# Kernel tuning notes

Measured on AMD Instinct MI355X. Metric: run time of the kernel, lower is better.

The kernel has to match this reference:

```python
import jax, jax.numpy as jnp
import numpy as np

N = 100000
E = 1600000
G = 256
D_IN = 128
NEURON = 64
ATT_F = 8
K = 3
ALPHA = 0.1


def setup_inputs() -> dict:
    key = jax.random.key(0)
    ks = jax.random.split(key, 12)
    x = jax.random.normal(ks[0], (N, D_IN), dtype=jnp.float32)
    closeness_feature = jax.random.normal(ks[1], (N, ATT_F), dtype=jnp.float32)
    edge_index = jax.random.randint(ks[2], (2, E), 0, N, dtype=jnp.int32)
    batch = jnp.sort(jax.random.randint(ks[3], (N,), 0, G, dtype=jnp.int32))
    s = 0.05
    return {
        "x": x,
        "closeness_feature": closeness_feature,
        "edge_index": edge_index,
        "batch": batch,
        "num_graphs": G,
        "nn1_w": jax.random.normal(ks[4], (D_IN, NEURON), dtype=jnp.float32) * s,
        "nn1_b": jnp.zeros((NEURON,), dtype=jnp.float32),
        "close_w": jax.random.normal(ks[5], (ATT_F, 1), dtype=jnp.float32) * s,
        "close_b": jnp.zeros((1,), dtype=jnp.float32),
        "att1_w": jax.random.normal(ks[6], (NEURON, 16), dtype=jnp.float32) * s,
        "att1_b": jnp.zeros((16,), dtype=jnp.float32),
        "att2_w": jax.random.normal(ks[7], (16, 1), dtype=jnp.float32) * s,
        "att2_b": jnp.zeros((1,), dtype=jnp.float32),
    }


def _appnp(x, edge_index, n):
    # gcn_norm with self-loops: A_hat = D^{-1/2}(A+I)D^{-1/2}
    loop = jnp.arange(n, dtype=edge_index.dtype)
    src = jnp.concatenate([edge_index[0], loop])
    dst = jnp.concatenate([edge_index[1], loop])
    deg = jax.ops.segment_sum(jnp.ones_like(dst, dtype=x.dtype), dst, num_segments=n)
    dinv = jax.lax.rsqrt(deg)  # deg >= 1 due to self loops
    norm = (dinv[src] * dinv[dst])[:, None]  # [E+N, 1]
    h = x
    for _ in range(K):
        agg = jax.ops.segment_sum(norm * h[src], dst, num_segments=n)
        h = (1.0 - ALPHA) * agg + ALPHA * x
    return h


def reference(x, closeness_feature, edge_index, batch, num_graphs,
              nn1_w, nn1_b, close_w, close_b, att1_w, att1_b, att2_w, att2_b):
    n = x.shape[0]
    h = _appnp(x, edge_index, n)                      # [N, D_IN]
    h = jax.nn.relu(h @ nn1_w + nn1_b)                # [N, 64]

    # per-graph softmax over closeness scores (segment softmax)
    logits = (closeness_feature @ close_w + close_b)[:, 0]          # [N]
    m = jax.ops.segment_max(logits, batch, num_segments=num_graphs)  # [G]
    w = jnp.exp(logits - m[batch])
    z = jax.ops.segment_sum(w, batch, num_segments=num_graphs)       # [G]
    p = w / z[batch]                                                 # softmax per graph

    cnt = jax.ops.segment_sum(jnp.ones((n,), dtype=h.dtype), batch,
                              num_segments=num_graphs)               # nodes per graph
    p = p * cnt[batch]                                               # scaled by curr_size

    # self_max: per-graph max over weighted node features
    pooled = jax.ops.segment_max(p[:, None] * h, batch, num_segments=num_graphs)  # [G, 64]

    a = jax.nn.relu(pooled @ att1_w + att1_b)         # [G, 16]
    return a @ att2_w + att2_b                        # [G, 1]
```

## Files before the change

### kernel.cpp

```cpp
#include <hip/hip_runtime.h>
#include <cstdint>
#include <cstddef>


#define DIN 128
#define NEU 64
#define BK2 512
#define BKSHIFT2 9
#define BKCAP 16384
#define ESCAP 12288
#define MAXNB 256

typedef __attribute__((ext_vector_type(8))) short short8v;
typedef __attribute__((ext_vector_type(4))) float f32x4;

__device__ inline float bf2f(unsigned short h) {
    return __uint_as_float(((unsigned)h) << 16);
}
__device__ inline unsigned short f2bf(float f) {
    unsigned u = __float_as_uint(f);
    unsigned r = u + 0x7FFFu + ((u >> 16) & 1u);
    return (unsigned short)(r >> 16);
}


__global__ __launch_bounds__(256) void binA_kernel(
        const int* __restrict__ src, const int* __restrict__ dst,
        int* __restrict__ bcur, int* __restrict__ pk, int E, int NB) {
    __shared__ int hist[MAXNB];
    __shared__ int cur[MAXNB];
    int nchunk = gridDim.x;
    int chunk = (E + nchunk - 1) / nchunk;
    int lo = blockIdx.x * chunk;
    int hi = min(E, lo + chunk);
    int t = threadIdx.x;
    for (int b = t; b < NB; b += 256) hist[b] = 0;
    __syncthreads();
    for (int i = lo + t; i < hi; i += 256)
        atomicAdd(&hist[dst[i] >> BKSHIFT2], 1);
    __syncthreads();
    for (int b = t; b < NB; b += 256)
        cur[b] = atomicAdd(&bcur[b], hist[b]);
    __syncthreads();
    for (int i = lo + t; i < hi; i += 256) {
        int d = dst[i];
        int b = d >> BKSHIFT2;
        int pos = atomicAdd(&cur[b], 1);
        pk[(size_t)b * BKCAP + pos] = (src[i] << BKSHIFT2) | (d & (BK2 - 1));
    }
}


__global__ void bscan_kernel(const int* __restrict__ bcur, int* __restrict__ bbase, int NB) {
    __shared__ int sh[256];
    int t = threadIdx.x;
    sh[t] = (t < NB) ? bcur[t] : 0;
    __syncthreads();
    for (int d = 1; d < 256; d <<= 1) {
        int v = (t >= d) ? sh[t - d] : 0;
        __syncthreads();
        sh[t] += v;
        __syncthreads();
    }
    if (t < NB) bbase[t + 1] = sh[t];
    if (t == 0) bbase[0] = 0;
}


__global__ __launch_bounds__(256) void binB_kernel(
        const int* __restrict__ bcur, const int* __restrict__ bbase,
        const int* __restrict__ pk, int* __restrict__ es,
        int* __restrict__ rowptr, float* __restrict__ dinv, int N, int NB) {
    __shared__ int cur[BK2];
    __shared__ int sh[256];
    __shared__ int esl[ESCAP];
    int b = blockIdx.x;
    int t = threadIdx.x;
    int node0 = b << BKSHIFT2;
    int count = bcur[b];
    int base = bbase[b];
    const int* pb = pk + (size_t)b * BKCAP;

    for (int v = t; v < BK2; v += 256) cur[v] = 0;
    __syncthreads();
    for (int i = t; i < count; i += 256)
        atomicAdd(&cur[pb[i] & (BK2 - 1)], 1);
    __syncthreads();
    int c0 = cur[2 * t], c1 = cur[2 * t + 1];
    int s = c0 + c1;
    sh[t] = s;
    __syncthreads();
    for (int d = 1; d < 256; d <<= 1) {
        int v = (t >= d) ? sh[t - d] : 0;
        __syncthreads();
        sh[t] += v;
        __syncthreads();
    }
    int excl = sh[t] - s;
    int n0 = node0 + 2 * t;
    if (n0 < N) {
        rowptr[n0 + 1] = base + excl + c0;
        dinv[n0] = rsqrtf((float)c0 + 1.0f);
    }
    if (n0 + 1 < N) {
        rowptr[n0 + 2] = base + excl + c0 + c1;
        dinv[n0 + 1] = rsqrtf((float)c1 + 1.0f);
    }
    if (b == 0 && t == 0) rowptr[0] = 0;
    __syncthreads();
    cur[2 * t] = excl;
    cur[2 * t + 1] = excl + c0;
    __syncthreads();
    for (int i = t; i < count; i += 256) {
        int v = pb[i];
        int pos = atomicAdd(&cur[v & (BK2 - 1)], 1);
        if (pos < ESCAP) esl[pos] = v >> BKSHIFT2;
    }
    __syncthreads();
    for (int i = t; i < count; i += 256) es[base + i] = esl[i];
}


__global__ __launch_bounds__(256) void fc1_kernel(
        const float* __restrict__ x, const float* __restrict__ W,
        const float* __restrict__ dinv, ushort* __restrict__ yb,
        ushort* __restrict__ g0, ushort* __restrict__ g1,
        ushort* __restrict__ g2, int N) {
    int tid = threadIdx.x;
    if (blockIdx.x == 0 && tid < 48) {
        int buf = tid >> 4, e = tid & 15;
        ushort* gp = (buf == 0) ? g0 : (buf == 1) ? g1 : g2;
        ((ushort4*)(gp + (size_t)N * NEU))[e] = make_ushort4(0, 0, 0, 0);
    }
    __shared__ ushort sW[DIN * NEU];
    for (int k = tid; k < DIN * NEU / 2; k += 256) {
        float2 v = ((const float2*)W)[k];
        ushort2 o;
        o.x = f2bf(v.x);
        o.y = f2bf(v.y);
        ((ushort2*)sW)[k] = o;
    }
    __syncthreads();
    int lane = tid & 63;
    int wv = tid >> 6;
    int l15 = lane & 15;
    int lg = lane >> 4;
    short8v bfrag[4][4];
#pragma unroll
    for (int kt = 0; kt < 4; kt++)
#pragma unroll
        for (int ct = 0; ct < 4; ct++) {
            short8v f;
#pragma unroll
            for (int e = 0; e < 8; e++)
                f[e] = (short)sW[(kt * 32 + lg * 8 + e) * NEU + ct * 16 + l15];
            bfrag[kt][ct] = f;
        }
    long long row0 = (long long)blockIdx.x * 64 + wv * 16;
    if (row0 >= N) return;
    bool rowok = (row0 + l15) < N;
    const float* xr = x + (size_t)(row0 + l15) * DIN;
    f32x4 acc[4];
#pragma unroll
    for (int ct = 0; ct < 4; ct++) acc[ct] = (f32x4){0.f, 0.f, 0.f, 0.f};
#pragma unroll
    for (int kt = 0; kt < 4; kt++) {
        short8v af = (short8v){0, 0, 0, 0, 0, 0, 0, 0};
        if (rowok) {
            float4 v0 = *((const float4*)(xr + kt * 32 + lg * 8));
            float4 v1 = *((const float4*)(xr + kt * 32 + lg * 8 + 4));
            af[0] = (short)f2bf(v0.x); af[1] = (short)f2bf(v0.y);
            af[2] = (short)f2bf(v0.z); af[3] = (short)f2bf(v0.w);
            af[4] = (short)f2bf(v1.x); af[5] = (short)f2bf(v1.y);
            af[6] = (short)f2bf(v1.z); af[7] = (short)f2bf(v1.w);
        }
#pragma unroll
        for (int ct = 0; ct < 4; ct++)
            acc[ct] = __builtin_amdgcn_mfma_f32_16x16x32_bf16(af, bfrag[kt][ct], acc[ct], 0, 0, 0);
    }
#pragma unroll
    for (int r = 0; r < 4; r++) {
        long long rr = row0 + lg * 4 + r;
        if (rr < N) {
            float dv = dinv[rr];
#pragma unroll
            for (int ct = 0; ct < 4; ct++) {
                float v = acc[ct][r];
                yb[(size_t)rr * NEU + ct * 16 + l15] = f2bf(v);
                g0[(size_t)rr * NEU + ct * 16 + l15] = f2bf(dv * v);
            }
        }
    }
}


template <int MODE>
__global__ __launch_bounds__(256) void pull_kernel(
        const int* __restrict__ rowptr, const int* __restrict__ es,
        const float* __restrict__ dinv, const ushort* __restrict__ gin,
        const ushort* __restrict__ yb, const float* __restrict__ b1,
        ushort* __restrict__ gout, float* __restrict__ h2out, int N) {
    int wid = threadIdx.x >> 6;
    int lane = threadIdx.x & 63;
    int quarter = lane >> 4;
    int l16 = lane & 15;
    int node = blockIdx.x * 4 + wid;
    if (node >= N) return;
    int beg = rowptr[node], end = rowptr[node + 1];
    float dd = dinv[node];
    const ushort4* gin4 = (const ushort4*)gin;
    float4 a0 = make_float4(0.f, 0.f, 0.f, 0.f);
    float4 a1 = make_float4(0.f, 0.f, 0.f, 0.f);
    int deg = end - beg;
    for (int base = 0; base < deg; base += 64) {
        int myi = base + lane;
        int msrc = (myi < deg) ? es[beg + myi] : N;
        int cnt = min(64, deg - base);
        int quads = (cnt + 3) >> 2;
        int j = 0;
        for (; j + 1 < quads; j += 2) {
            int s0 = __shfl(msrc, 4 * j + quarter);
            int s1 = __shfl(msrc, 4 * j + 4 + quarter);
            ushort4 w0 = gin4[(uint)(s0 << 4) + l16];
            ushort4 w1 = gin4[(uint)(s1 << 4) + l16];
            a0.x += bf2f(w0.x); a0.y += bf2f(w0.y); a0.z += bf2f(w0.z); a0.w += bf2f(w0.w);
            a1.x += bf2f(w1.x); a1.y += bf2f(w1.y); a1.z += bf2f(w1.z); a1.w += bf2f(w1.w);
        }
        if (j < quads) {
            int s0 = __shfl(msrc, 4 * j + quarter);
            ushort4 w0 = gin4[(uint)(s0 << 4) + l16];
            a0.x += bf2f(w0.x); a0.y += bf2f(w0.y); a0.z += bf2f(w0.z); a0.w += bf2f(w0.w);
        }
    }
    float4 acc;
    acc.x = a0.x + a1.x;
    acc.y = a0.y + a1.y;
    acc.z = a0.z + a1.z;
    acc.w = a0.w + a1.w;
    acc.x += __shfl_xor(acc.x, 16);
    acc.y += __shfl_xor(acc.y, 16);
    acc.z += __shfl_xor(acc.z, 16);
    acc.w += __shfl_xor(acc.w, 16);
    acc.x += __shfl_xor(acc.x, 32);
    acc.y += __shfl_xor(acc.y, 32);
    acc.z += __shfl_xor(acc.z, 32);
    acc.w += __shfl_xor(acc.w, 32);
    if (quarter == 0) {
        ushort4 gv = *((const ushort4*)(gin + (size_t)node * NEU) + l16);
        ushort4 yv = *((const ushort4*)(yb + (size_t)node * NEU) + l16);
        float c9 = 0.9f * dd;
        float hx = c9 * (acc.x + bf2f(gv.x)) + 0.1f * bf2f(yv.x);
        float hy = c9 * (acc.y + bf2f(gv.y)) + 0.1f * bf2f(yv.y);
        float hz = c9 * (acc.z + bf2f(gv.z)) + 0.1f * bf2f(yv.z);
        float hw = c9 * (acc.w + bf2f(gv.w)) + 0.1f * bf2f(yv.w);
        if (MODE == 1) {
            float4 bb = *((const float4*)b1 + l16);
            float4 o;
            o.x = fmaxf(hx + bb.x, 0.f);
            o.y = fmaxf(hy + bb.y, 0.f);
            o.z = fmaxf(hz + bb.z, 0.f);
            o.w = fmaxf(hw + bb.w, 0.f);
            *((float4*)(h2out + (size_t)node * NEU) + l16) = o;
        } else {
            ushort4 o;
            o.x = f2bf(dd * hx); o.y = f2bf(dd * hy);
            o.z = f2bf(dd * hz); o.w = f2bf(dd * hw);
            *((ushort4*)(gout + (size_t)node * NEU) + l16) = o;
        }
    }
}


__global__ __launch_bounds__(256) void head_kernel(
        const int* __restrict__ batch, const float* __restrict__ cf,
        const float* __restrict__ cw, const float* __restrict__ cb,
        const float* __restrict__ h2, const float* __restrict__ aw1,
        const float* __restrict__ ab1, const float* __restrict__ aw2,
        const float* __restrict__ ab2, float* __restrict__ out, int N) {
    int g = blockIdx.x;
    int tid = threadIdx.x;
    __shared__ int sbound[2];
    __shared__ float redm[256];
    __shared__ float redz[256];
    __shared__ float pooled[64];
    __shared__ float sa[16];
    if (tid < 2) {
        int target = g + tid;
        int lo = 0, hi = N;
        while (lo < hi) {
            int mid = (lo + hi) >> 1;
            if (batch[mid] < target) lo = mid + 1; else hi = mid;
        }
        sbound[tid] = lo;
    }
    __syncthreads();
    int s0 = sbound[0], e0 = sbound[1];
    float w0 = cw[0], w1 = cw[1], w2 = cw[2], w3 = cw[3];
    float w4 = cw[4], w5 = cw[5], w6 = cw[6], w7 = cw[7];
    float cb0 = cb[0];
    float m = -INFINITY, z = 0.f;
    for (int i = s0 + tid; i < e0; i += 256) {
        const float4* c = (const float4*)(cf + (size_t)i * 8);
        float4 A = c[0], B = c[1];
        float l = A.x * w0 + A.y * w1 + A.z * w2 + A.w * w3
                + B.x * w4 + B.y * w5 + B.z * w6 + B.w * w7 + cb0;
        float mn = fmaxf(m, l);
        z = z * __expf(m - mn) + __expf(l - mn);
        m = mn;
    }
    redm[tid] = m; redz[tid] = z;
    __syncthreads();
    for (int w = 128; w > 0; w >>= 1) {
        if (tid < w) {
            float ma = redm[tid], mb = redm[tid + w];
            float za = redz[tid], zb = redz[tid + w];
            float mn = fmaxf(ma, mb);
            redz[tid] = (mn == -INFINITY) ? 0.f
                       : za * __expf(ma - mn) + zb * __expf(mb - mn);
            redm[tid] = mn;
        }
        __syncthreads();
    }
    float M = redm[0];
    float scale = (float)(e0 - s0) / redz[0];
    __syncthreads();
    int j = tid & 63, r = tid >> 6;
    float mx = -INFINITY;
    for (int i = s0 + r; i < e0; i += 4) {
        const float4* c = (const float4*)(cf + (size_t)i * 8);
        float4 A = c[0], B = c[1];
        float l = A.x * w0 + A.y * w1 + A.z * w2 + A.w * w3
                + B.x * w4 + B.y * w5 + B.z * w6 + B.w * w7 + cb0;
        float p = __expf(l - M) * scale;
        mx = fmaxf(mx, p * h2[(size_t)i * NEU + j]);
    }
    redm[tid] = mx;
    __syncthreads();
    if (r == 0)
        pooled[j] = fmaxf(fmaxf(redm[j], redm[64 + j]),
                          fmaxf(redm[128 + j], redm[192 + j]));
    __syncthreads();
    if (tid < 16) {
        float acc = ab1[tid];
#pragma unroll
        for (int k = 0; k < 64; k++) acc = fmaf(pooled[k], aw1[k * 16 + tid], acc);
        sa[tid] = fmaxf(acc, 0.f);
    }
    __syncthreads();
    if (tid == 0) {
        float o = ab2[0];
#pragma unroll
        for (int k = 0; k < 16; k++) o = fmaf(sa[k], aw2[k], o);
        out[g] = o;
    }
}


extern "C" void kernel_launch(void* const* d_in, const int* in_sizes, int n_in,
                              void* d_out, int out_size, void* d_ws, size_t ws_size,
                              hipStream_t stream) {
    const float* x       = (const float*)d_in[0];
    const float* cf      = (const float*)d_in[1];
    const int*   ei      = (const int*)d_in[2];
    const int*   batch   = (const int*)d_in[3];
    const float* nn1_w   = (const float*)d_in[5];
    const float* nn1_b   = (const float*)d_in[6];
    const float* close_w = (const float*)d_in[7];
    const float* close_b = (const float*)d_in[8];
    const float* att1_w  = (const float*)d_in[9];
    const float* att1_b  = (const float*)d_in[10];
    const float* att2_w  = (const float*)d_in[11];
    const float* att2_b  = (const float*)d_in[12];
    float* out = (float*)d_out;

    int N = in_sizes[0] / DIN;
    int E = in_sizes[2] / 2;
    int G = out_size;

    const int* src = ei;
    const int* dst = ei + E;

    char* w = (char*)d_ws;
    size_t off = 0;
    auto alloc = [&](size_t bytes) -> void* {
        void* ptr = w + off;
        off += (bytes + 511) & ~(size_t)511;
        return ptr;
    };
    int NB = (N + BK2 - 1) >> BKSHIFT2;

    ushort* yb     = (ushort*)alloc((size_t)N * NEU * 2);
    ushort* g0     = (ushort*)alloc(((size_t)N + 1) * NEU * 2);
    ushort* g1     = (ushort*)alloc(((size_t)N + 1) * NEU * 2);
    ushort* g2     = (ushort*)alloc(((size_t)N + 1) * NEU * 2);
    float* h2      = (float*)alloc((size_t)N * NEU * 4);
    float* dinv    = (float*)alloc((size_t)N * 4);
    int*   rowptr  = (int*)alloc(((size_t)N + 1) * 4);
    int*   es      = (int*)alloc((size_t)E * 4);
    int*   bcur    = (int*)alloc((size_t)NB * 4);
    int*   bbase   = (int*)alloc(((size_t)NB + 1) * 4);
    int*   pk      = (int*)alloc((size_t)NB * BKCAP * 4);
    (void)ws_size; (void)n_in;

    hipMemsetAsync(bcur, 0, (size_t)NB * 4, stream);

    binA_kernel<<<256, 256, 0, stream>>>(src, dst, bcur, pk, E, NB);
    bscan_kernel<<<1, 256, 0, stream>>>(bcur, bbase, NB);
    binB_kernel<<<NB, 256, 0, stream>>>(bcur, bbase, pk, es, rowptr, dinv, N, NB);

    fc1_kernel<<<(N + 63) / 64, 256, 0, stream>>>(x, nn1_w, dinv, yb, g0, g1, g2, N);

    pull_kernel<0><<<(N + 3) / 4, 256, 0, stream>>>(rowptr, es, dinv, g0, yb, nn1_b, g1, nullptr, N);
    pull_kernel<0><<<(N + 3) / 4, 256, 0, stream>>>(rowptr, es, dinv, g1, yb, nn1_b, g2, nullptr, N);
    pull_kernel<1><<<(N + 3) / 4, 256, 0, stream>>>(rowptr, es, dinv, g2, yb, nn1_b, nullptr, h2, N);

    head_kernel<<<G, 256, 0, stream>>>(batch, cf, close_w, close_b, h2,
                                       att1_w, att1_b, att2_w, att2_b, out, N);
}
```

Baseline: 242.7 us.

## Stage binned edges in LDS, fold bucket scan into binB, unroll pull by four

binA now computes a local prefix over its bucket histogram and stages packed edges in shared memory sorted by bucket. It then writes them to global memory in bucket-contiguous runs, aiming for more coalesced scattered writes. The separate bscan kernel is removed and every binB block recomputes the prefix over bucket counts itself, which saves one launch at the cost of redundant scans. The pull kernel's gather loop is unrolled to four independent loads and accumulators for more memory-level parallelism. The risk is that ASTAGE=6400 must cover the per-block chunk (E/256=6250), and the extra shared memory may reduce occupancy.

```diff
diff --git a/kernel.cpp b/kernel.cpp
--- a/kernel.cpp
+++ b/kernel.cpp
@@ -10,6 +10,7 @@
 #define BKCAP 16384
 #define ESCAP 12288
 #define MAXNB 256
+#define ASTAGE 6400
 
 typedef __attribute__((ext_vector_type(8))) short short8v;
 typedef __attribute__((ext_vector_type(4))) float f32x4;
@@ -28,7 +29,12 @@
         const int* __restrict__ src, const int* __restrict__ dst,
         int* __restrict__ bcur, int* __restrict__ pk, int E, int NB) {
     __shared__ int hist[MAXNB];
-    __shared__ int cur[MAXNB];
+    __shared__ int lstart[MAXNB];
+    __shared__ int lcur[MAXNB];
+    __shared__ int resv[MAXNB];
+    __shared__ int sh[256];
+    __shared__ int stage[ASTAGE];
+    __shared__ int gidx[ASTAGE];
     int nchunk = gridDim.x;
     int chunk = (E + nchunk - 1) / nchunk;
     int lo = blockIdx.x * chunk;
@@ -39,61 +45,75 @@
     for (int i = lo + t; i < hi; i += 256)
         atomicAdd(&hist[dst[i] >> BKSHIFT2], 1);
     __syncthreads();
-    for (int b = t; b < NB; b += 256)
-        cur[b] = atomicAdd(&bcur[b], hist[b]);
+    int c = (t < NB) ? hist[t] : 0;
+    sh[t] = c;
+    __syncthreads();
+    for (int d = 1; d < 256; d <<= 1) {
+        int u = (t >= d) ? sh[t - d] : 0;
+        __syncthreads();
+        sh[t] += u;
+        __syncthreads();
+    }
+    if (t < NB) {
+        int excl = sh[t] - c;
+        lstart[t] = excl;
+        lcur[t] = excl;
+        resv[t] = atomicAdd(&bcur[t], c);
+    }
     __syncthreads();
     for (int i = lo + t; i < hi; i += 256) {
-        int d = dst[i];
-        int b = d >> BKSHIFT2;
-        int pos = atomicAdd(&cur[b], 1);
-        pk[(size_t)b * BKCAP + pos] = (src[i] << BKSHIFT2) | (d & (BK2 - 1));
-    }
-}
-
-
-__global__ void bscan_kernel(const int* __restrict__ bcur, int* __restrict__ bbase, int NB) {
-    __shared__ int sh[256];
-    int t = threadIdx.x;
-    sh[t] = (t < NB) ? bcur[t] : 0;
-    __syncthreads();
-    for (int d = 1; d < 256; d <<= 1) {
-        int v = (t >= d) ? sh[t - d] : 0;
-        __syncthreads();
-        sh[t] += v;
-        __syncthreads();
-    }
-    if (t < NB) bbase[t + 1] = sh[t];
-    if (t == 0) bbase[0] = 0;
+        int d = dst[i], b = d >> BKSHIFT2;
+        int p = atomicAdd(&lcur[b], 1);
+        stage[p] = (src[i] << BKSHIFT2) | (d & (BK2 - 1));
+        gidx[p] = resv[b] + (p - lstart[b]) + b * BKCAP;
+    }
+    __syncthreads();
+    int total = hi - lo;
+    for (int q = t; q < total; q += 256)
+        pk[gidx[q]] = stage[q];
 }
 
 
 __global__ __launch_bounds__(256) void binB_kernel(
-        const int* __restrict__ bcur, const int* __restrict__ bbase,
-        const int* __restrict__ pk, int* __restrict__ es,
-        int* __restrict__ rowptr, float* __restrict__ dinv, int N, int NB) {
+        const int* __restrict__ bcur, const int* __restrict__ pk,
+        int* __restrict__ es, int* __restrict__ rowptr,
+        float* __restrict__ dinv, int N, int NB) {
     __shared__ int cur[BK2];
     __shared__ int sh[256];
     __shared__ int esl[ESCAP];
+    __shared__ int sbase[2];
     int b = blockIdx.x;
     int t = threadIdx.x;
     int node0 = b << BKSHIFT2;
-    int count = bcur[b];
-    int base = bbase[b];
+    int v = (t < NB) ? bcur[t] : 0;
+    sh[t] = v;
+    __syncthreads();
+    for (int d = 1; d < 256; d <<= 1) {
+        int u = (t >= d) ? sh[t - d] : 0;
+        __syncthreads();
+        sh[t] += u;
+        __syncthreads();
+    }
+    if (t == b) { sbase[0] = sh[t] - v; sbase[1] = v; }
+    __syncthreads();
+    int base = sbase[0];
+    int count = sbase[1];
     const int* pb = pk + (size_t)b * BKCAP;
 
-    for (int v = t; v < BK2; v += 256) cur[v] = 0;
+    for (int q = t; q < BK2; q += 256) cur[q] = 0;
     __syncthreads();
     for (int i = t; i < count; i += 256)
         atomicAdd(&cur[pb[i] & (BK2 - 1)], 1);
     __syncthreads();
     int c0 = cur[2 * t], c1 = cur[2 * t + 1];
     int s = c0 + c1;
+    __syncthreads();
     sh[t] = s;
     __syncthreads();
     for (int d = 1; d < 256; d <<= 1) {
-        int v = (t >= d) ? sh[t - d] : 0;
-        __syncthreads();
-        sh[t] += v;
+        int u = (t >= d) ? sh[t - d] : 0;
+        __syncthreads();
+        sh[t] += u;
         __syncthreads();
     }
     int excl = sh[t] - s;
@@ -112,9 +132,9 @@
     cur[2 * t + 1] = excl + c0;
     __syncthreads();
     for (int i = t; i < count; i += 256) {
-        int v = pb[i];
-        int pos = atomicAdd(&cur[v & (BK2 - 1)], 1);
-        if (pos < ESCAP) esl[pos] = v >> BKSHIFT2;
+        int w = pb[i];
+        int pos = atomicAdd(&cur[w & (BK2 - 1)], 1);
+        if (pos < ESCAP) esl[pos] = w >> BKSHIFT2;
     }
     __syncthreads();
     for (int i = t; i < count; i += 256) es[base + i] = esl[i];
@@ -193,6 +213,10 @@
     }
 }
 
+
+__device__ inline void acc4(float4& a, ushort4 w) {
+    a.x += bf2f(w.x); a.y += bf2f(w.y); a.z += bf2f(w.z); a.w += bf2f(w.w);
+}
 
 template <int MODE>
 __global__ __launch_bounds__(256) void pull_kernel(
@@ -211,6 +235,8 @@
     const ushort4* gin4 = (const ushort4*)gin;
     float4 a0 = make_float4(0.f, 0.f, 0.f, 0.f);
     float4 a1 = make_float4(0.f, 0.f, 0.f, 0.f);
+    float4 a2 = make_float4(0.f, 0.f, 0.f, 0.f);
+    float4 a3 = make_float4(0.f, 0.f, 0.f, 0.f);
     int deg = end - beg;
     for (int base = 0; base < deg; base += 64) {
         int myi = base + lane;
@@ -218,25 +244,28 @@
         int cnt = min(64, deg - base);
         int quads = (cnt + 3) >> 2;
         int j = 0;
-        for (; j + 1 < quads; j += 2) {
+        for (; j + 3 < quads; j += 4) {
             int s0 = __shfl(msrc, 4 * j + quarter);
             int s1 = __shfl(msrc, 4 * j + 4 + quarter);
+            int s2 = __shfl(msrc, 4 * j + 8 + quarter);
+            int s3 = __shfl(msrc, 4 * j + 12 + quarter);
             ushort4 w0 = gin4[(uint)(s0 << 4) + l16];
             ushort4 w1 = gin4[(uint)(s1 << 4) + l16];
-            a0.x += bf2f(w0.x); a0.y += bf2f(w0.y); a0.z += bf2f(w0.z); a0.w += bf2f(w0.w);
-            a1.x += bf2f(w1.x); a1.y += bf2f(w1.y); a1.z += bf2f(w1.z); a1.w += bf2f(w1.w);
-        }
-        if (j < quads) {
+            ushort4 w2 = gin4[(uint)(s2 << 4) + l16];
+            ushort4 w3 = gin4[(uint)(s3 << 4) + l16];
+            acc4(a0, w0); acc4(a1, w1); acc4(a2, w2); acc4(a3, w3);
+        }
+        for (; j < quads; j++) {
             int s0 = __shfl(msrc, 4 * j + quarter);
             ushort4 w0 = gin4[(uint)(s0 << 4) + l16];
-            a0.x += bf2f(w0.x); a0.y += bf2f(w0.y); a0.z += bf2f(w0.z); a0.w += bf2f(w0.w);
+            acc4(a0, w0);
         }
     }
     float4 acc;
-    acc.x = a0.x + a1.x;
-    acc.y = a0.y + a1.y;
-    acc.z = a0.z + a1.z;
-    acc.w = a0.w + a1.w;
+    acc.x = (a0.x + a1.x) + (a2.x + a3.x);
+    acc.y = (a0.y + a1.y) + (a2.y + a3.y);
+    acc.z = (a0.z + a1.z) + (a2.z + a3.z);
+    acc.w = (a0.w + a1.w) + (a2.w + a3.w);
     acc.x += __shfl_xor(acc.x, 16);
     acc.y += __shfl_xor(acc.y, 16);
     acc.z += __shfl_xor(acc.z, 16);
@@ -398,15 +427,13 @@
     int*   rowptr  = (int*)alloc(((size_t)N + 1) * 4);
     int*   es      = (int*)alloc((size_t)E * 4);
     int*   bcur    = (int*)alloc((size_t)NB * 4);
-    int*   bbase   = (int*)alloc(((size_t)NB + 1) * 4);
     int*   pk      = (int*)alloc((size_t)NB * BKCAP * 4);
     (void)ws_size; (void)n_in;
 
     hipMemsetAsync(bcur, 0, (size_t)NB * 4, stream);
 
     binA_kernel<<<256, 256, 0, stream>>>(src, dst, bcur, pk, E, NB);
-    bscan_kernel<<<1, 256, 0, stream>>>(bcur, bbase, NB);
-    binB_kernel<<<NB, 256, 0, stream>>>(bcur, bbase, pk, es, rowptr, dinv, N, NB);
+    binB_kernel<<<NB, 256, 0, stream>>>(bcur, pk, es, rowptr, dinv, N, NB);
 
     fc1_kernel<<<(N + 63) / 64, 256, 0, stream>>>(x, nn1_w, dinv, yb, g0, g1, g2, N);
 
```

After: 238.4 us. About the same (-1.8%).
